# Kernel optimization log

Hardware: AMD Instinct MI355X
Metric: run time of the kernel (lower is better)

## Reference

```python
import jax, jax.numpy as jnp
import numpy as np


def _hard_sigmoid(x):
    # Keras ConvLSTM2D default recurrent_activation
    return jnp.clip(0.2 * x + 0.5, 0.0, 1.0)


def _conv(x, w):
    # NHWC input, HWIO kernel, SAME padding, stride 1
    return jax.lax.conv_general_dilated(
        x, w, (1, 1), 'SAME', dimension_numbers=('NHWC', 'HWIO', 'NHWC'))


def _convlstm(seq, h, c, k, rk, b):
    # seq: [B, T, H, W, Cin]; h, c: [B, H, W, F]
    # k: [kh, kw, Cin, 4F], rk: [kh, kw, F, 4F], b: [4F]
    def step(carry, x):
        h, c = carry
        z = _conv(x, k) + _conv(h, rk) + b  # [B,H,W,4F]
        zi, zf, zc, zo = jnp.split(z, 4, axis=-1)
        i = _hard_sigmoid(zi)
        f = _hard_sigmoid(zf)
        o = _hard_sigmoid(zo)
        c = f * c + i * jnp.tanh(zc)
        h = o * jnp.tanh(c)
        return (h, c), None
    (h, c), _ = jax.lax.scan(step, (h, c), jnp.swapaxes(seq, 0, 1))
    return h, c


def setup_inputs() -> dict:
    key = jax.random.key(0)
    ks = jax.random.split(key, 14)
    B, T, H, W, Cin, F, K = 32, 1, 64, 64, 1, 64, 3
    s = 0.05
    inp = {
        'input_': jax.random.normal(ks[0], (B, T, H, W, Cin), jnp.float32),
        'h0': jax.random.normal(ks[1], (B, H, W, F), jnp.float32) * s,
        'c0': jax.random.normal(ks[2], (B, H, W, F), jnp.float32) * s,
        'h1': jax.random.normal(ks[3], (B, H, W, F), jnp.float32) * s,
        'c1': jax.random.normal(ks[4], (B, H, W, F), jnp.float32) * s,
        'k0': jax.random.normal(ks[5], (K, K, Cin, 4 * F), jnp.float32) * s,
        'rk0': jax.random.normal(ks[6], (K, K, F, 4 * F), jnp.float32) * s,
        'b0': jnp.zeros((4 * F,), jnp.float32),
        'k1': jax.random.normal(ks[7], (K, K, F, 4 * F), jnp.float32) * s,
        'rk1': jax.random.normal(ks[8], (K, K, F, 4 * F), jnp.float32) * s,
        'b1': jnp.zeros((4 * F,), jnp.float32),
        'cw': jax.random.normal(ks[9], (1, 1, F, 1), jnp.float32) * s,
        'cb': jnp.zeros((1,), jnp.float32),
    }
    return inp


def reference(input_, h0, c0, h1, c1, k0, rk0, b0, k1, rk1, b1, cw, cb):
    # Layer 0 consumes the input frame sequence (T=1)
    h0n, c0n = _convlstm(input_, h0, c0, k0, rk0, b0)
    # Layer 1 consumes layer-0's last hidden state as its (length-1) input
    h1n, c1n = _convlstm(h0n[:, None], h1, c1, k1, rk1, b1)
    frames = _conv(h1n, cw) + cb  # 1x1 conv head -> [B,H,W,1]
    return frames, h0n, c0n, h1n, c1n
```

## Files before the change

kernel.cpp:

```cpp
#include <hip/hip_runtime.h>
#include <hip/hip_bf16.h>

typedef short s16;
typedef __attribute__((ext_vector_type(8))) short bf16x8;
typedef __attribute__((ext_vector_type(4))) float f32x4;

__device__ __forceinline__ s16 f2bf(float f) {
  unsigned u = __builtin_bit_cast(unsigned, f);
  unsigned r = (u + 0x7FFFu + ((u >> 16) & 1u)) >> 16;
  return (s16)r;
}

__device__ __forceinline__ float hsig(float x) {
  return fminf(fmaxf(0.2f * x + 0.5f, 0.0f), 1.0f);
}

#define PXS 66
#define ROWSZ (PXS * 64)
#define ASZ6 (6 * ROWSZ)

__global__ void wprep_kernel(const float* __restrict__ rk0, const float* __restrict__ k1,
                             const float* __restrict__ rk1, const float* __restrict__ k0,
                             s16* __restrict__ w0q, s16* __restrict__ w1q,
                             s16* __restrict__ w2q, s16* __restrict__ k0t) {
  int idx = blockIdx.x * 256 + threadIdx.x;
  const int n1 = 18 * 8192;
  if (idx < 3 * n1) {
    int which = idx / n1;
    int i = idx - which * n1;
    int e    = i & 7;
    int lane = (i >> 3) & 63;
    int g    = (i >> 9) & 3;
    int j    = (i >> 11) & 3;
    int k    = (i >> 13) & 1;
    int tap  = i >> 14;
    int l15 = lane & 15, l4 = lane >> 4;
    int ic = k * 32 + l4 * 8 + e;
    int oc = j * 64 + g * 16 + l15;
    const float* src = (which == 0) ? rk0 : (which == 1) ? k1 : rk1;
    s16* dst = (which == 0) ? w0q : (which == 1) ? w1q : w2q;
    dst[i] = f2bf(src[(tap * 64 + ic) * 256 + oc]);
  } else if (idx < 3 * n1 + 8192) {
    int r = idx - 3 * n1;
    int kk = r & 31;
    int oc = r >> 5;
    k0t[r] = (kk < 9) ? f2bf(k0[kk * 256 + oc]) : (s16)0;
  }
}

template <bool F32>
__device__ __forceinline__ bf16x8 load_conv8(const void* src, long off) {
  if constexpr (F32) {
    const float* p = (const float*)src + off;
    float4 v0 = *reinterpret_cast<const float4*>(p);
    float4 v1 = *reinterpret_cast<const float4*>(p + 4);
    bf16x8 r;
    r[0] = f2bf(v0.x); r[1] = f2bf(v0.y); r[2] = f2bf(v0.z); r[3] = f2bf(v0.w);
    r[4] = f2bf(v1.x); r[5] = f2bf(v1.y); r[6] = f2bf(v1.z); r[7] = f2bf(v1.w);
    return r;
  } else {
    return *reinterpret_cast<const bf16x8*>((const s16*)src + off);
  }
}

template <bool F32>
__device__ __forceinline__ void stage6(s16* a_lds, const void* src, int b, int y0, int tid) {
  #pragma unroll
  for (int i = 0; i < 3; ++i) {
    int c   = tid + i * 1024;
    int row = c >> 9;
    int px  = (c >> 3) & 63;
    int cb  = c & 7;
    int y   = y0 - 1 + row;
    int xp  = px + 1;
    bf16x8 v = {};
    if ((unsigned)y < 64u)
      v = load_conv8<F32>(src, ((long)(b * 64 + y) * 64 + px) * 64 + cb * 8);
    *reinterpret_cast<bf16x8*>(a_lds + (row * PXS + xp) * 64 + ((cb ^ (xp & 7)) * 8)) = v;
  }
  if (tid < 96) {
    int row = tid >> 4;
    int xp  = ((tid >> 3) & 1) ? 65 : 0;
    int cb  = tid & 7;
    bf16x8 z = {};
    *reinterpret_cast<bf16x8*>(a_lds + (row * PXS + xp) * 64 + cb * 8) = z;
  }
}

template <int NSRC, bool XPATH, bool S0F32, bool S1F32>
__global__ __launch_bounds__(1024, 1) void cell_kernel(
    const void* __restrict__ src0,
    const void* __restrict__ src1,
    const s16* __restrict__ w0,
    const s16* __restrict__ w1,
    const float* __restrict__ xin,
    const s16* __restrict__ k0t,
    const float* __restrict__ bias,
    const float* __restrict__ c_old,
    float* __restrict__ h_out,
    float* __restrict__ c_out,
    s16* __restrict__ hb_out)
{
  __shared__ __align__(16) s16 a_lds[NSRC * ASZ6];
  __shared__ __align__(16) s16 w_lds[3][8192];
  __shared__ float x_lds[XPATH ? 384 : 1];

  const int tid = threadIdx.x;
  const int b  = blockIdx.x >> 4;
  const int y0 = (blockIdx.x & 15) << 2;

  const int wave = tid >> 6;
  const int lane = tid & 63;
  const int g    = wave & 3;
  const int mh   = wave >> 2;
  const int l15  = lane & 15;
  const int l4   = lane >> 4;

  constexpr int NST = NSRC * 18;

  auto issueW = [&](int u) {
    int v = (u >= NST) ? u - NST : u;
    int si = (NSRC == 2 && v >= 18) ? 1 : 0;
    int vv = v - 18 * si;
    const s16* wt = (si ? w1 : w0) + vv * 8192;
    char* base = (char*)(&w_lds[0][0]) + (v % 3) * 16384 + (tid >> 6) * 1024;
    __builtin_amdgcn_global_load_lds(
        (const __attribute__((address_space(1))) void*)(wt + tid * 8),
        (__attribute__((address_space(3))) void*)base, 16, 0, 0);
  };

  auto readWf = [&](bf16x8 (&wf)[4], int slot) {
    const s16* wb = &w_lds[slot][0] + g * 512 + lane * 8;
    #pragma unroll
    for (int j = 0; j < 4; ++j)
      wf[j] = *reinterpret_cast<const bf16x8*>(wb + j * 2048);
  };

  f32x4 acc[4][4] = {};

  auto doStage = [&](const bf16x8 (&wf)[4], int u) {
    int si = (NSRC == 2 && u >= 18) ? 1 : 0;
    int uu = u - 18 * si;
    int tap = uu >> 1, kk = uu & 1;
    int dy = tap / 3, dx = tap - dy * 3;
    const char* sb = (const char*)a_lds + si * (ASZ6 * 2) + (mh + dy) * (ROWSZ * 2);
    bf16x8 af[4];
    #pragma unroll
    for (int m = 0; m < 4; ++m) {
      int xq   = m * 16 + l15 + dx;
      int boff = xq * 128 + ((((kk << 2) | l4) ^ (xq & 7)) << 4);
      af[m] = *reinterpret_cast<const bf16x8*>(sb + boff);
    }
    __builtin_amdgcn_s_setprio(1);
    #pragma unroll
    for (int m = 0; m < 4; ++m) {
      #pragma unroll
      for (int j = 0; j < 4; ++j)
        acc[m][j] = __builtin_amdgcn_mfma_f32_16x16x32_bf16(af[m], wf[j], acc[m][j], 0, 0, 0);
    }
    __builtin_amdgcn_s_setprio(0);
  };

  issueW(0);
  issueW(1);
  stage6<S0F32>(a_lds, src0, b, y0, tid);
  if (NSRC == 2) stage6<S1F32>(a_lds + ASZ6, src1, b, y0, tid);
  if (XPATH) {
    if (tid < 384) {
      int row = tid >> 6, px = tid & 63;
      int y = y0 - 1 + row;
      x_lds[tid] = ((unsigned)y < 64u) ? xin[(b * 64 + y) * 64 + px] : 0.0f;
    }
  }
  __syncthreads();

  if (XPATH) {
    bf16x8 bx[4];
    #pragma unroll
    for (int j = 0; j < 4; ++j) {
      int oc = j * 64 + g * 16 + l15;
      bx[j] = *reinterpret_cast<const bf16x8*>(k0t + oc * 32 + l4 * 8);
    }
    #pragma unroll
    for (int m = 0; m < 4; ++m) {
      int px = m * 16 + l15;
      bf16x8 ax = {};
      #pragma unroll
      for (int e = 0; e < 8; ++e) {
        int t = l4 * 8 + e;
        if (t < 9) {
          int dyt = t / 3, dxt = t - dyt * 3;
          int xx = px + dxt - 1;
          float xv = ((unsigned)xx < 64u) ? x_lds[(mh + dyt) * 64 + xx] : 0.0f;
          ax[e] = f2bf(xv);
        }
      }
      #pragma unroll
      for (int j = 0; j < 4; ++j)
        acc[m][j] = __builtin_amdgcn_mfma_f32_16x16x32_bf16(ax, bx[j], acc[m][j], 0, 0, 0);
    }
  }

  bf16x8 wf[4];
  #pragma unroll
  for (int u = 0; u < NST; ++u) {
    asm volatile("s_waitcnt vmcnt(1)" ::: "memory");
    __builtin_amdgcn_s_barrier();
    __builtin_amdgcn_sched_barrier(0);
    issueW(u + 2);
    readWf(wf, u % 3);
    doStage(wf, u);
  }

  float bi[4];
  #pragma unroll
  for (int j = 0; j < 4; ++j) bi[j] = bias[j * 64 + g * 16 + l15];

  const int pix_base = b * 4096 + y0 * 64;
  const int f = g * 16 + l15;
  #pragma unroll
  for (int m = 0; m < 4; ++m) {
    #pragma unroll
    for (int r = 0; r < 4; ++r) {
      int pl = mh * 64 + m * 16 + l4 * 4 + r;
      int off = (pix_base + pl) * 64 + f;
      float zi = acc[m][0][r] + bi[0];
      float zf = acc[m][1][r] + bi[1];
      float zc = acc[m][2][r] + bi[2];
      float zo = acc[m][3][r] + bi[3];
      float ig = hsig(zi), fg = hsig(zf), og = hsig(zo);
      float cn = fg * c_old[off] + ig * tanhf(zc);
      float hn = og * tanhf(cn);
      c_out[off] = cn;
      h_out[off] = hn;
      if (hb_out) hb_out[off] = f2bf(hn);
    }
  }
}

__global__ void frames_kernel(const float* __restrict__ h, const float* __restrict__ cw,
                              const float* __restrict__ cbp, float* __restrict__ out) {
  int tid = blockIdx.x * 256 + threadIdx.x;
  int p  = tid >> 2;
  int fc = (tid & 3) * 16;
  const float4* hp = reinterpret_cast<const float4*>(h + p * 64 + fc);
  const float4* wp = reinterpret_cast<const float4*>(cw + fc);
  float s = 0.0f;
  #pragma unroll
  for (int i = 0; i < 4; ++i) {
    float4 v = hp[i];
    float4 w = wp[i];
    s += v.x * w.x + v.y * w.y + v.z * w.z + v.w * w.w;
  }
  s += __shfl_xor(s, 1);
  s += __shfl_xor(s, 2);
  if ((tid & 3) == 0) out[p] = s + cbp[0];
}

extern "C" void kernel_launch(void* const* d_in, const int* in_sizes, int n_in,
                              void* d_out, int out_size, void* d_ws, size_t ws_size,
                              hipStream_t stream) {
  const float* x   = (const float*)d_in[0];
  const float* h0  = (const float*)d_in[1];
  const float* c0  = (const float*)d_in[2];
  const float* h1  = (const float*)d_in[3];
  const float* c1  = (const float*)d_in[4];
  const float* k0  = (const float*)d_in[5];
  const float* rk0 = (const float*)d_in[6];
  const float* b0  = (const float*)d_in[7];
  const float* k1  = (const float*)d_in[8];
  const float* rk1 = (const float*)d_in[9];
  const float* b1  = (const float*)d_in[10];
  const float* cw  = (const float*)d_in[11];
  const float* cbp = (const float*)d_in[12];

  float* out    = (float*)d_out;
  float* frames = out;
  float* h0n    = out + 131072;
  float* c0n    = out + 131072 + 8388608;
  float* h1n    = out + 131072 + 2 * 8388608;
  float* c1n    = out + 131072 + 3 * 8388608;

  char* ws = (char*)d_ws;
  const size_t SZ_H = 16777216;
  s16* h0nb = (s16*)(ws + 0 * SZ_H);
  s16* w0q  = (s16*)(ws + 1 * SZ_H);
  s16* w1q  = (s16*)(ws + 1 * SZ_H + 1 * 294912);
  s16* w2q  = (s16*)(ws + 1 * SZ_H + 2 * 294912);
  s16* k0t  = (s16*)(ws + 1 * SZ_H + 3 * 294912);

  wprep_kernel<<<1760, 256, 0, stream>>>(rk0, k1, rk1, k0, w0q, w1q, w2q, k0t);

  cell_kernel<1, true, true, false><<<512, 1024, 0, stream>>>(
      h0, nullptr, w0q, nullptr, x, k0t, b0, c0, h0n, c0n, h0nb);

  cell_kernel<2, false, false, true><<<512, 1024, 0, stream>>>(
      h0nb, h1, w1q, w2q, nullptr, nullptr, b1, c1, h1n, c1n, nullptr);

  frames_kernel<<<2048, 256, 0, stream>>>(h1n, cw, cbp, frames);
}
```

Measured before the change: 185.5 us.

## Split cell kernel into producer weight-loader waves and consumer MFMA waves

```diff
diff --git a/kernel.cpp b/kernel.cpp
--- a/kernel.cpp
+++ b/kernel.cpp
@@ -17,7 +17,7 @@
 
 #define PXS 66
 #define ROWSZ (PXS * 64)
-#define ASZ6 (6 * ROWSZ)
+#define ASZ4 (4 * ROWSZ)
 
 __global__ void wprep_kernel(const float* __restrict__ rk0, const float* __restrict__ k1,
                              const float* __restrict__ rk1, const float* __restrict__ k0,
@@ -64,10 +64,10 @@
 }
 
 template <bool F32>
-__device__ __forceinline__ void stage6(s16* a_lds, const void* src, int b, int y0, int tid) {
+__device__ __forceinline__ void stage4(s16* a_lds, const void* src, int b, int y0, int tid) {
   #pragma unroll
-  for (int i = 0; i < 3; ++i) {
-    int c   = tid + i * 1024;
+  for (int i = 0; i < 4; ++i) {
+    int c   = tid + i * 512;
     int row = c >> 9;
     int px  = (c >> 3) & 63;
     int cb  = c & 7;
@@ -78,7 +78,7 @@
       v = load_conv8<F32>(src, ((long)(b * 64 + y) * 64 + px) * 64 + cb * 8);
     *reinterpret_cast<bf16x8*>(a_lds + (row * PXS + xp) * 64 + ((cb ^ (xp & 7)) * 8)) = v;
   }
-  if (tid < 96) {
+  if (tid < 64) {
     int row = tid >> 4;
     int xp  = ((tid >> 3) & 1) ? 65 : 0;
     int cb  = tid & 7;
@@ -88,7 +88,7 @@
 }
 
 template <int NSRC, bool XPATH, bool S0F32, bool S1F32>
-__global__ __launch_bounds__(1024, 1) void cell_kernel(
+__global__ __launch_bounds__(640, 1) void cell_kernel(
     const void* __restrict__ src0,
     const void* __restrict__ src1,
     const s16* __restrict__ w0,
@@ -101,139 +101,152 @@
     float* __restrict__ c_out,
     s16* __restrict__ hb_out)
 {
-  __shared__ __align__(16) s16 a_lds[NSRC * ASZ6];
+  __shared__ __align__(16) s16 a_lds[NSRC * ASZ4];
   __shared__ __align__(16) s16 w_lds[3][8192];
-  __shared__ float x_lds[XPATH ? 384 : 1];
+  __shared__ float x_lds[XPATH ? 256 : 1];
 
   const int tid = threadIdx.x;
-  const int b  = blockIdx.x >> 4;
-  const int y0 = (blockIdx.x & 15) << 2;
+  const int b  = blockIdx.x >> 5;
+  const int y0 = (blockIdx.x & 31) << 1;
 
   const int wave = tid >> 6;
   const int lane = tid & 63;
-  const int g    = wave & 3;
-  const int mh   = wave >> 2;
-  const int l15  = lane & 15;
-  const int l4   = lane >> 4;
 
   constexpr int NST = NSRC * 18;
 
   auto issueW = [&](int u) {
-    int v = (u >= NST) ? u - NST : u;
-    int si = (NSRC == 2 && v >= 18) ? 1 : 0;
-    int vv = v - 18 * si;
-    const s16* wt = (si ? w1 : w0) + vv * 8192;
-    char* base = (char*)(&w_lds[0][0]) + (v % 3) * 16384 + (tid >> 6) * 1024;
-    __builtin_amdgcn_global_load_lds(
-        (const __attribute__((address_space(1))) void*)(wt + tid * 8),
-        (__attribute__((address_space(3))) void*)base, 16, 0, 0);
+    int si = (NSRC == 2 && u >= 18) ? 1 : 0;
+    const s16* wt = (si ? w1 : w0) + (u - 18 * si) * 8192;
+    char* slot = (char*)(&w_lds[0][0]) + (u % 3) * 16384 + (wave - 8) * 1024;
+    #pragma unroll
+    for (int i = 0; i < 8; ++i)
+      __builtin_amdgcn_global_load_lds(
+          (const __attribute__((address_space(1))) void*)(wt + (i * 128 + (wave - 8) * 64) * 8 + lane * 8),
+          (__attribute__((address_space(3))) void*)(slot + i * 2048), 16, 0, 0);
   };
 
-  auto readWf = [&](bf16x8 (&wf)[4], int slot) {
-    const s16* wb = &w_lds[slot][0] + g * 512 + lane * 8;
-    #pragma unroll
-    for (int j = 0; j < 4; ++j)
-      wf[j] = *reinterpret_cast<const bf16x8*>(wb + j * 2048);
-  };
-
-  f32x4 acc[4][4] = {};
-
-  auto doStage = [&](const bf16x8 (&wf)[4], int u) {
-    int si = (NSRC == 2 && u >= 18) ? 1 : 0;
-    int uu = u - 18 * si;
-    int tap = uu >> 1, kk = uu & 1;
-    int dy = tap / 3, dx = tap - dy * 3;
-    const char* sb = (const char*)a_lds + si * (ASZ6 * 2) + (mh + dy) * (ROWSZ * 2);
-    bf16x8 af[4];
+  if (wave >= 8) {
+    issueW(0);
+    issueW(1);
+  } else {
+    stage4<S0F32>(a_lds, src0, b, y0, tid);
+    if (NSRC == 2) stage4<S1F32>(a_lds + ASZ4, src1, b, y0, tid);
+    if (XPATH) {
+      if (tid < 256) {
+        int row = tid >> 6, px = tid & 63;
+        int y = y0 - 1 + row;
+        x_lds[tid] = ((unsigned)y < 64u) ? xin[(b * 64 + y) * 64 + px] : 0.0f;
+      }
+    }
+  }
+  __syncthreads();
+
+  if (wave < 8) {
+    const int g   = wave & 3;
+    const int mh  = wave >> 2;
+    const int l15 = lane & 15;
+    const int l4  = lane >> 4;
+
+    f32x4 acc[4][4] = {};
+
+    if (XPATH) {
+      bf16x8 bx[4];
+      #pragma unroll
+      for (int j = 0; j < 4; ++j) {
+        int oc = j * 64 + g * 16 + l15;
+        bx[j] = *reinterpret_cast<const bf16x8*>(k0t + oc * 32 + l4 * 8);
+      }
+      #pragma unroll
+      for (int m = 0; m < 4; ++m) {
+        int px = m * 16 + l15;
+        bf16x8 ax = {};
+        #pragma unroll
+        for (int e = 0; e < 8; ++e) {
+          int t = l4 * 8 + e;
+          if (t < 9) {
+            int dyt = t / 3, dxt = t - dyt * 3;
+            int xx = px + dxt - 1;
+            float xv = ((unsigned)xx < 64u) ? x_lds[(mh + dyt) * 64 + xx] : 0.0f;
+            ax[e] = f2bf(xv);
+          }
+        }
+        #pragma unroll
+        for (int j = 0; j < 4; ++j)
+          acc[m][j] = __builtin_amdgcn_mfma_f32_16x16x32_bf16(ax, bx[j], acc[m][j], 0, 0, 0);
+      }
+    }
+
+    auto readWf = [&](bf16x8 (&wf)[4], int slot) {
+      const s16* wb = &w_lds[slot][0] + g * 512 + lane * 8;
+      #pragma unroll
+      for (int j = 0; j < 4; ++j)
+        wf[j] = *reinterpret_cast<const bf16x8*>(wb + j * 2048);
+    };
+    auto doStage = [&](const bf16x8 (&wf)[4], int u) {
+      int si = (NSRC == 2 && u >= 18) ? 1 : 0;
+      int uu = u - 18 * si;
+      int tap = uu >> 1, kk = uu & 1;
+      int dy = tap / 3, dx = tap - dy * 3;
+      const char* lb = (const char*)a_lds + (si * ASZ4 + (mh + dy) * ROWSZ) * 2;
+      bf16x8 af[4];
+      #pragma unroll
+      for (int m = 0; m < 4; ++m) {
+        int xq   = m * 16 + l15 + dx;
+        int boff = xq * 128 + ((((kk << 2) | l4) ^ (xq & 7)) << 4);
+        af[m] = *reinterpret_cast<const bf16x8*>(lb + boff);
+      }
+      __builtin_amdgcn_s_setprio(1);
+      #pragma unroll
+      for (int m = 0; m < 4; ++m) {
+        #pragma unroll
+        for (int j = 0; j < 4; ++j)
+          acc[m][j] = __builtin_amdgcn_mfma_f32_16x16x32_bf16(af[m], wf[j], acc[m][j], 0, 0, 0);
+      }
+      __builtin_amdgcn_s_setprio(0);
+    };
+
+    bf16x8 wf[4];
+    #pragma unroll
+    for (int u = 0; u < NST; ++u) {
+      __builtin_amdgcn_s_barrier();
+      readWf(wf, u % 3);
+      doStage(wf, u);
+    }
+
+    float bi[4];
+    #pragma unroll
+    for (int j = 0; j < 4; ++j) bi[j] = bias[j * 64 + g * 16 + l15];
+
+    const int pix_base = b * 4096 + y0 * 64;
+    const int f = g * 16 + l15;
     #pragma unroll
     for (int m = 0; m < 4; ++m) {
-      int xq   = m * 16 + l15 + dx;
-      int boff = xq * 128 + ((((kk << 2) | l4) ^ (xq & 7)) << 4);
-      af[m] = *reinterpret_cast<const bf16x8*>(sb + boff);
-    }
-    __builtin_amdgcn_s_setprio(1);
-    #pragma unroll
-    for (int m = 0; m < 4; ++m) {
-      #pragma unroll
-      for (int j = 0; j < 4; ++j)
-        acc[m][j] = __builtin_amdgcn_mfma_f32_16x16x32_bf16(af[m], wf[j], acc[m][j], 0, 0, 0);
-    }
-    __builtin_amdgcn_s_setprio(0);
-  };
-
-  issueW(0);
-  issueW(1);
-  stage6<S0F32>(a_lds, src0, b, y0, tid);
-  if (NSRC == 2) stage6<S1F32>(a_lds + ASZ6, src1, b, y0, tid);
-  if (XPATH) {
-    if (tid < 384) {
-      int row = tid >> 6, px = tid & 63;
-      int y = y0 - 1 + row;
-      x_lds[tid] = ((unsigned)y < 64u) ? xin[(b * 64 + y) * 64 + px] : 0.0f;
-    }
-  }
-  __syncthreads();
-
-  if (XPATH) {
-    bf16x8 bx[4];
-    #pragma unroll
-    for (int j = 0; j < 4; ++j) {
-      int oc = j * 64 + g * 16 + l15;
-      bx[j] = *reinterpret_cast<const bf16x8*>(k0t + oc * 32 + l4 * 8);
-    }
-    #pragma unroll
-    for (int m = 0; m < 4; ++m) {
-      int px = m * 16 + l15;
-      bf16x8 ax = {};
-      #pragma unroll
-      for (int e = 0; e < 8; ++e) {
-        int t = l4 * 8 + e;
-        if (t < 9) {
-          int dyt = t / 3, dxt = t - dyt * 3;
-          int xx = px + dxt - 1;
-          float xv = ((unsigned)xx < 64u) ? x_lds[(mh + dyt) * 64 + xx] : 0.0f;
-          ax[e] = f2bf(xv);
-        }
-      }
-      #pragma unroll
-      for (int j = 0; j < 4; ++j)
-        acc[m][j] = __builtin_amdgcn_mfma_f32_16x16x32_bf16(ax, bx[j], acc[m][j], 0, 0, 0);
-    }
-  }
-
-  bf16x8 wf[4];
-  #pragma unroll
-  for (int u = 0; u < NST; ++u) {
-    asm volatile("s_waitcnt vmcnt(1)" ::: "memory");
-    __builtin_amdgcn_s_barrier();
-    __builtin_amdgcn_sched_barrier(0);
-    issueW(u + 2);
-    readWf(wf, u % 3);
-    doStage(wf, u);
-  }
-
-  float bi[4];
-  #pragma unroll
-  for (int j = 0; j < 4; ++j) bi[j] = bias[j * 64 + g * 16 + l15];
-
-  const int pix_base = b * 4096 + y0 * 64;
-  const int f = g * 16 + l15;
-  #pragma unroll
-  for (int m = 0; m < 4; ++m) {
-    #pragma unroll
-    for (int r = 0; r < 4; ++r) {
-      int pl = mh * 64 + m * 16 + l4 * 4 + r;
-      int off = (pix_base + pl) * 64 + f;
-      float zi = acc[m][0][r] + bi[0];
-      float zf = acc[m][1][r] + bi[1];
-      float zc = acc[m][2][r] + bi[2];
-      float zo = acc[m][3][r] + bi[3];
-      float ig = hsig(zi), fg = hsig(zf), og = hsig(zo);
-      float cn = fg * c_old[off] + ig * tanhf(zc);
-      float hn = og * tanhf(cn);
-      c_out[off] = cn;
-      h_out[off] = hn;
-      if (hb_out) hb_out[off] = f2bf(hn);
+      #pragma unroll
+      for (int r = 0; r < 4; ++r) {
+        int pl = mh * 64 + m * 16 + l4 * 4 + r;
+        int off = (pix_base + pl) * 64 + f;
+        float zi = acc[m][0][r] + bi[0];
+        float zf = acc[m][1][r] + bi[1];
+        float zc = acc[m][2][r] + bi[2];
+        float zo = acc[m][3][r] + bi[3];
+        float ig = hsig(zi), fg = hsig(zf), og = hsig(zo);
+        float cn = fg * c_old[off] + ig * tanhf(zc);
+        float hn = og * tanhf(cn);
+        c_out[off] = cn;
+        h_out[off] = hn;
+        if (hb_out) hb_out[off] = f2bf(hn);
+      }
+    }
+  } else {
+    #pragma unroll
+    for (int u = 0; u < NST; ++u) {
+      if (u + 2 < NST) {
+        issueW(u + 2);
+        asm volatile("s_waitcnt vmcnt(8)" ::: "memory");
+      } else {
+        asm volatile("s_waitcnt vmcnt(0)" ::: "memory");
+      }
+      __builtin_amdgcn_s_barrier();
     }
   }
 }
@@ -291,10 +304,10 @@
 
   wprep_kernel<<<1760, 256, 0, stream>>>(rk0, k1, rk1, k0, w0q, w1q, w2q, k0t);
 
-  cell_kernel<1, true, true, false><<<512, 1024, 0, stream>>>(
+  cell_kernel<1, true, true, false><<<1024, 640, 0, stream>>>(
       h0, nullptr, w0q, nullptr, x, k0t, b0, c0, h0n, c0n, h0nb);
 
-  cell_kernel<2, false, false, true><<<512, 1024, 0, stream>>>(
+  cell_kernel<2, false, false, true><<<1024, 640, 0, stream>>>(
       h0nb, h1, w1q, w2q, nullptr, nullptr, b1, c1, h1n, c1n, nullptr);
 
   frames_kernel<<<2048, 256, 0, stream>>>(h1n, cw, cbp, frames);
```

Measured after the change: 212.4 us. 14.5% more time.
